# Optimization experiments

Measured on AMD Instinct MI355X. Metric: run time of the kernel, lower is better.

The kernel has to match this reference:

```python
import jax, jax.numpy as jnp
import numpy as np

E = 128
H = 4
D = E // H  # head dim = 32
NEG = -1e9


def setup_inputs() -> dict:
    key = jax.random.key(0)
    ks = jax.random.split(key, 4)
    B, N = 8, 2048
    x = jax.random.normal(ks[0], (B, N, E), dtype=jnp.float32)
    adj = jax.random.randint(ks[1], (B, N, N), 0, 2, dtype=jnp.int32)
    # nn.MultiheadAttention params: packed in_proj (3E,E) + out_proj (E,E)
    in_proj_w = jax.random.normal(ks[2], (3 * E, E), dtype=jnp.float32) * (1.0 / np.sqrt(E))
    in_proj_b = jnp.zeros((3 * E,), dtype=jnp.float32)
    out_w = jax.random.normal(ks[3], (E, E), dtype=jnp.float32) * (1.0 / np.sqrt(E))
    out_b = jnp.zeros((E,), dtype=jnp.float32)
    return {"x": x, "adj": adj, "in_proj_w": in_proj_w, "in_proj_b": in_proj_b,
            "out_w": out_w, "out_b": out_b}


def reference(x, adj, in_proj_w, in_proj_b, out_w, out_b):
    B, N, _ = x.shape
    # additive mask from FIRST batch element only (as in the torch module)
    mask = jnp.where(adj[0] == 0, jnp.float32(NEG), jnp.float32(0.0))  # (N,N)
    # packed QKV projection: x @ W^T + b
    qkv = x @ in_proj_w.T + in_proj_b  # (B,N,3E)
    q, k, v = jnp.split(qkv, 3, axis=-1)
    # (B,N,E) -> (B,H,N,D)
    def heads(t):
        return t.reshape(B, N, H, D).transpose(0, 2, 1, 3)
    q, k, v = heads(q), heads(k), heads(v)
    scores = jnp.einsum('bhnd,bhmd->bhnm', q, k) / jnp.sqrt(jnp.float32(D))
    scores = scores + mask[None, None]  # broadcast shared mask
    attn = jax.nn.softmax(scores, axis=-1)
    out = jnp.einsum('bhnm,bhmd->bhnd', attn, v)  # (B,H,N,D)
    out = out.transpose(0, 2, 1, 3).reshape(B, N, E)
    return out @ out_w.T + out_b
```

## Files before the change

### kernel.cpp

```cpp
#include <hip/hip_runtime.h>


#define EDIM 128
#define SCALE2 0.25503483f
#define COFF  -5.7707801f

typedef unsigned int uint32;
typedef float f32x4 __attribute__((ext_vector_type(4)));
typedef short s16x8 __attribute__((ext_vector_type(8)));
typedef _Float16 f16x2 __attribute__((ext_vector_type(2)));
typedef _Float16 f16x4 __attribute__((ext_vector_type(4)));
typedef _Float16 f16x8 __attribute__((ext_vector_type(8)));
typedef __fp16 g16x2 __attribute__((ext_vector_type(2)));

__device__ inline float bf2f(ushort u) { return __uint_as_float(((uint32)u) << 16); }
__device__ inline ushort f2bf(float f) {
  uint32 u = __float_as_uint(f);
  u += 0x7fffu + ((u >> 16) & 1u);
  return (ushort)(u >> 16);
}
__device__ inline uint32 packbf(float a, float b) {
  uint32 ua = __float_as_uint(a) + 0x8000u;
  uint32 ub = __float_as_uint(b) + 0x8000u;
  return __builtin_amdgcn_perm(ub, ua, 0x07060302u);
}
__device__ inline f16x2 pkrtz(float a, float b) {
  g16x2 t = __builtin_amdgcn_cvt_pkrtz(a, b);
  return __builtin_bit_cast(f16x2, t);
}
__device__ inline float fexp2(float x) {
#if __has_builtin(__builtin_amdgcn_exp2f)
  return __builtin_amdgcn_exp2f(x);
#else
  return __exp2f(x);
#endif
}

__device__ inline f32x4 mfma32(s16x8 a, s16x8 b, f32x4 c) {
  return __builtin_amdgcn_mfma_f32_16x16x32_bf16(a, b, c, 0, 0, 0);
}
__device__ inline f32x4 mfma32h(f16x8 a, f16x8 b, f32x4 c) {
  return __builtin_amdgcn_mfma_f32_16x16x32_f16(a, b, c, 0, 0, 0);
}

#if __has_builtin(__builtin_amdgcn_global_load_lds)
#define HAVE_GLL 1
__device__ inline void gll16(const void* g, void* l) {
  __builtin_amdgcn_global_load_lds(
      (const __attribute__((address_space(1))) unsigned int*)g,
      (__attribute__((address_space(3))) unsigned int*)l, 16, 0, 0);
}
#else
#define HAVE_GLL 0
#endif

__device__ inline int sniff_fp32(const ushort* __restrict__ xus) {
  int lane = threadIdx.x & 63, cnt = 0;
#pragma unroll
  for (int i = 0; i < 4; i++) {
    ushort v = xus[2 * (lane * 4 + i)];
    int ex = (v >> 7) & 0xFF;
    cnt += (ex >= 100 && ex <= 140) ? 1 : 0;
  }
#pragma unroll
  for (int s = 1; s < 64; s <<= 1) cnt += __shfl_xor(cnt, s);
  return cnt < 128;
}

__device__ inline s16x8 load8(const void* p, size_t e, int fp32) {
  if (fp32) {
    const float* f = (const float*)p + e;
    float4 lo = *(const float4*)f;
    float4 hi = *(const float4*)(f + 4);
    union { s16x8 s; uint32 u[4]; } r;
    r.u[0] = packbf(lo.x, lo.y);
    r.u[1] = packbf(lo.z, lo.w);
    r.u[2] = packbf(hi.x, hi.y);
    r.u[3] = packbf(hi.z, hi.w);
    return r.s;
  }
  return *(const s16x8*)((const ushort*)p + e);
}
__device__ inline float loads(const void* p, size_t e, int fp32) {
  return fp32 ? ((const float*)p)[e] : bf2f(((const ushort*)p)[e]);
}

__global__ __launch_bounds__(256) void k_mask(const int4* __restrict__ adj4,
                                              uint32* __restrict__ mb) {
  int g = blockIdx.x * 256 + threadIdx.x;
  int4 v = adj4[g];
  int lane = threadIdx.x & 63;
  uint32 nib = (v.x != 0 ? 1u : 0u) | (v.y != 0 ? 2u : 0u) |
               (v.z != 0 ? 4u : 0u) | (v.w != 0 ? 8u : 0u);
  uint32 w = nib << (4 * (lane & 7));
  w |= __shfl_xor(w, 1);
  w |= __shfl_xor(w, 2);
  w |= __shfl_xor(w, 4);
  if ((lane & 7) == 0) mb[g >> 3] = w;
}

__global__ __launch_bounds__(256) void k_qkv(const void* __restrict__ x,
                                             const void* __restrict__ w,
                                             const void* __restrict__ bias,
                                             ushort* __restrict__ Qg,
                                             ushort* __restrict__ Kg,
                                             _Float16* __restrict__ Vth) {
  const int fp32 = sniff_fp32((const ushort*)x);
  const int tid = threadIdx.x;
  const int wave = tid >> 6, lane = tid & 63, L = lane & 15, quad = lane >> 4;
  const int mt = blockIdx.x * 64 + wave * 16;
  const int jt0 = blockIdx.y * 8;

  s16x8 a[4];
#pragma unroll
  for (int ks = 0; ks < 4; ks++)
    a[ks] = load8(x, (size_t)(mt + L) * EDIM + ks * 32 + quad * 8, fp32);

  const int bidx = mt >> 11;
  const int npos0 = (mt & 2047) + quad * 4;

  for (int jj = 0; jj < 8; jj++) {
    int jt = jt0 + jj;
    f32x4 acc = {0.f, 0.f, 0.f, 0.f};
#pragma unroll
    for (int ks = 0; ks < 4; ks++) {
      s16x8 bf = load8(w, (size_t)(jt * 16 + L) * EDIM + ks * 32 + quad * 8, fp32);
      acc = mfma32(a[ks], bf, acc);
    }
    int j = jt * 16 + L;
    float badd = loads(bias, j, fp32);
    int jm = j & 127;
    int h = jm >> 5, d = jm & 31;
    int bh = bidx * 4 + h;
    int ch = npos0 >> 7, kk = npos0 & 127;
    if (jt < 8) {
#pragma unroll
      for (int r = 0; r < 4; r++)
        Qg[(size_t)bh * 65536 + (size_t)(npos0 + r) * 32 + d] = f2bf((acc[r] + badd) * SCALE2);
    } else if (jt < 16) {
      int sub = kk >> 5, k32 = kk & 31, t = k32 >> 3, r8 = k32 & 7;
      int slot0 = sub * 32 + ((r8 >> 2) << 4) + t * 4;
      size_t kb = (size_t)bh * 65536 + (size_t)ch * 4096;
#pragma unroll
      for (int r = 0; r < 4; r++)
        Kg[kb + (size_t)(slot0 + r) * 32 + (((d >> 3) ^ r) << 3) + (d & 7)] =
            f2bf(acc[r] + badd);
    } else {
      int g = kk >> 3, e0 = kk & 7;
      f16x2 h0 = pkrtz(acc[0] + badd, acc[1] + badd);
      f16x2 h1 = pkrtz(acc[2] + badd, acc[3] + badd);
      f16x4 pk; pk[0] = h0[0]; pk[1] = h0[1]; pk[2] = h1[0]; pk[3] = h1[1];
      *(f16x4*)(Vth + (size_t)bh * 65536 + (size_t)ch * 4096 + d * 128 +
                (g ^ (d & 7)) * 8 + e0) = pk;
    }
  }
}

__global__ __launch_bounds__(256) void k_attn(const ushort* __restrict__ Qg,
                                              const ushort* __restrict__ Kg,
                                              const _Float16* __restrict__ Vth,
                                              const uint32* __restrict__ mb,
                                              const ushort* __restrict__ xus,
                                              ushort* Oglob, ushort* Oa) {
  __shared__ ushort Klds[2][128 * 32];
  __shared__ ushort Vlds[2][32 * 128];

  const int fp32 = sniff_fp32(xus);
  ushort* O = fp32 ? Oa : Oglob;

  const int tid = threadIdx.x;
  const int wv = tid >> 6, lane = tid & 63, L = lane & 15, quad = lane >> 4;
  const int bh = blockIdx.x >> 4;
  const int q0 = (blockIdx.x & 15) * 128 + wv * 32;
  const int qgA = q0 + L, qgB = q0 + 16 + L;

  const ushort* Qb = Qg + (size_t)bh * 65536;
  s16x8 qfA = *(const s16x8*)(Qb + (size_t)qgA * 32 + quad * 8);
  s16x8 qfB = *(const s16x8*)(Qb + (size_t)qgB * 32 + quad * 8);

  f32x4 OA0 = {0,0,0,0}, OA1 = {0,0,0,0}, OB0 = {0,0,0,0}, OB1 = {0,0,0,0};
  f32x4 LA = {0,0,0,0}, LB = {0,0,0,0};
  f16x8 ones;
#pragma unroll
  for (int i = 0; i < 8; i++) ones[i] = (_Float16)1.0f;

  const char* Kg8 = (const char*)(Kg + (size_t)bh * 65536);
  const char* Vg8 = (const char*)(Vth + (size_t)bh * 65536);
  const int g0 = quad ^ (L & 3);

#define STAGE(c, p)                                                          \
  do {                                                                       \
    _Pragma("unroll")                                                        \
    for (int j = 0; j < 2; j++) {                                            \
      int off = (wv + 4 * j) * 1024;                                         \
      gll16(Kg8 + (size_t)(c) * 8192 + off + lane * 16, (char*)Klds[p] + off);\
      gll16(Vg8 + (size_t)(c) * 8192 + off + lane * 16, (char*)Vlds[p] + off);\
    }                                                                        \
  } while (0)

#if HAVE_GLL
  STAGE(0, 0);
#else
#pragma unroll
  for (int r = 0; r < 2; r++) {
    int idx = r * 256 + tid;
    *(s16x8*)((char*)Klds[0] + idx * 16) = *(const s16x8*)(Kg8 + idx * 16);
    *(s16x8*)((char*)Vlds[0] + idx * 16) = *(const s16x8*)(Vg8 + idx * 16);
  }
#endif

  for (int c = 0; c < 16; c++) {
    const int p = c & 1;
    __syncthreads();
#if HAVE_GLL
    if (c + 1 < 16) STAGE(c + 1, 1 - p);
#else
    if (c + 1 < 16) {
#pragma unroll
      for (int r = 0; r < 2; r++) {
        int idx = r * 256 + tid;
        *(s16x8*)((char*)Klds[1 - p] + idx * 16) =
            *(const s16x8*)(Kg8 + (size_t)(c + 1) * 8192 + idx * 16);
        *(s16x8*)((char*)Vlds[1 - p] + idx * 16) =
            *(const s16x8*)(Vg8 + (size_t)(c + 1) * 8192 + idx * 16);
      }
    }
#endif

    uint4 mA = *(const uint4*)(mb + (size_t)qgA * 64 + c * 4);
    uint4 mB = *(const uint4*)(mb + (size_t)qgB * 64 + c * 4);
    uint32 mAw[4] = {mA.x, mA.y, mA.z, mA.w};
    uint32 mBw[4] = {mB.x, mB.y, mB.z, mB.w};

#pragma unroll
    for (int sub = 0; sub < 4; sub++) {
      const f32x4 Zc = {COFF, COFF, COFF, COFF};
      s16x8 kf0 = *(const s16x8*)&Klds[p][(sub * 32 + L) * 32 + g0 * 8];
      s16x8 kf1 = *(const s16x8*)&Klds[p][(sub * 32 + 16 + L) * 32 + g0 * 8];
      f32x4 sA0 = mfma32(kf0, qfA, Zc), sA1 = mfma32(kf1, qfA, Zc);
      f32x4 sB0 = mfma32(kf0, qfB, Zc), sB1 = mfma32(kf1, qfB, Zc);

      uint32 mwqA = mAw[sub] >> (quad * 8);
      uint32 mwqB = mBw[sub] >> (quad * 8);
      union { f16x8 v; f16x2 h[4]; } pA, pB;
      float a0 = ((mwqA >> 0) & 1u) ? fexp2(sA0[0]) : 0.f;
      float a1 = ((mwqA >> 1) & 1u) ? fexp2(sA0[1]) : 0.f;
      float a2 = ((mwqA >> 2) & 1u) ? fexp2(sA0[2]) : 0.f;
      float a3 = ((mwqA >> 3) & 1u) ? fexp2(sA0[3]) : 0.f;
      float a4 = ((mwqA >> 4) & 1u) ? fexp2(sA1[0]) : 0.f;
      float a5 = ((mwqA >> 5) & 1u) ? fexp2(sA1[1]) : 0.f;
      float a6 = ((mwqA >> 6) & 1u) ? fexp2(sA1[2]) : 0.f;
      float a7 = ((mwqA >> 7) & 1u) ? fexp2(sA1[3]) : 0.f;
      pA.h[0] = pkrtz(a0, a1); pA.h[1] = pkrtz(a2, a3);
      pA.h[2] = pkrtz(a4, a5); pA.h[3] = pkrtz(a6, a7);
      float b0 = ((mwqB >> 0) & 1u) ? fexp2(sB0[0]) : 0.f;
      float b1 = ((mwqB >> 1) & 1u) ? fexp2(sB0[1]) : 0.f;
      float b2 = ((mwqB >> 2) & 1u) ? fexp2(sB0[2]) : 0.f;
      float b3 = ((mwqB >> 3) & 1u) ? fexp2(sB0[3]) : 0.f;
      float b4 = ((mwqB >> 4) & 1u) ? fexp2(sB1[0]) : 0.f;
      float b5 = ((mwqB >> 5) & 1u) ? fexp2(sB1[1]) : 0.f;
      float b6 = ((mwqB >> 6) & 1u) ? fexp2(sB1[2]) : 0.f;
      float b7 = ((mwqB >> 7) & 1u) ? fexp2(sB1[3]) : 0.f;
      pB.h[0] = pkrtz(b0, b1); pB.h[1] = pkrtz(b2, b3);
      pB.h[2] = pkrtz(b4, b5); pB.h[3] = pkrtz(b6, b7);

      int g = (sub * 4 + quad) ^ (L & 7);
      f16x8 vf0 = *(const f16x8*)&Vlds[p][L * 128 + g * 8];
      f16x8 vf1 = *(const f16x8*)&Vlds[p][(16 + L) * 128 + g * 8];
      OA0 = mfma32h(vf0, pA.v, OA0);  OA1 = mfma32h(vf1, pA.v, OA1);
      OB0 = mfma32h(vf0, pB.v, OB0);  OB1 = mfma32h(vf1, pB.v, OB1);
      LA  = mfma32h(ones, pA.v, LA);  LB  = mfma32h(ones, pB.v, LB);
    }
  }

  int b = bh >> 2, h = bh & 3;
  {
    float rn = 1.0f / LA[0];
    size_t ob = ((size_t)(b * 2048 + qgA)) * 128 + h * 32 + quad * 4;
    ushort4 p0, p1;
    p0.x = f2bf(OA0[0] * rn); p0.y = f2bf(OA0[1] * rn);
    p0.z = f2bf(OA0[2] * rn); p0.w = f2bf(OA0[3] * rn);
    p1.x = f2bf(OA1[0] * rn); p1.y = f2bf(OA1[1] * rn);
    p1.z = f2bf(OA1[2] * rn); p1.w = f2bf(OA1[3] * rn);
    *(ushort4*)(O + ob) = p0; *(ushort4*)(O + ob + 16) = p1;
  }
  {
    float rn = 1.0f / LB[0];
    size_t ob = ((size_t)(b * 2048 + qgB)) * 128 + h * 32 + quad * 4;
    ushort4 p0, p1;
    p0.x = f2bf(OB0[0] * rn); p0.y = f2bf(OB0[1] * rn);
    p0.z = f2bf(OB0[2] * rn); p0.w = f2bf(OB0[3] * rn);
    p1.x = f2bf(OB1[0] * rn); p1.y = f2bf(OB1[1] * rn);
    p1.z = f2bf(OB1[2] * rn); p1.w = f2bf(OB1[3] * rn);
    *(ushort4*)(O + ob) = p0; *(ushort4*)(O + ob + 16) = p1;
  }
}

__global__ __launch_bounds__(256) void k_proj(void* outp, const ushort* Oa,
                                              const void* w, const void* bias,
                                              const ushort* __restrict__ xus) {
  const int fp32 = sniff_fp32(xus);
  const ushort* src = fp32 ? Oa : (const ushort*)outp;
  const int tid = threadIdx.x;
  const int wave = tid >> 6, lane = tid & 63, L = lane & 15, quad = lane >> 4;
  const int mt = blockIdx.x * 64 + wave * 16;

  s16x8 a[4];
#pragma unroll
  for (int ks = 0; ks < 4; ks++)
    a[ks] = *(const s16x8*)(src + (size_t)(mt + L) * EDIM + ks * 32 + quad * 8);

  for (int jt = 0; jt < 8; jt++) {
    f32x4 acc = {0.f, 0.f, 0.f, 0.f};
#pragma unroll
    for (int ks = 0; ks < 4; ks++) {
      s16x8 bf = load8(w, (size_t)(jt * 16 + L) * EDIM + ks * 32 + quad * 8, fp32);
      acc = mfma32(a[ks], bf, acc);
    }
    float badd = loads(bias, jt * 16 + L, fp32);
#pragma unroll
    for (int r = 0; r < 4; r++) {
      size_t idx = (size_t)(mt + quad * 4 + r) * EDIM + jt * 16 + L;
      if (fp32) ((float*)outp)[idx] = acc[r] + badd;
      else      ((ushort*)outp)[idx] = f2bf(acc[r] + badd);
    }
  }
}

extern "C" void kernel_launch(void* const* d_in, const int* in_sizes, int n_in,
                              void* d_out, int out_size, void* d_ws, size_t ws_size,
                              hipStream_t stream) {
  const void* x   = d_in[0];
  const int*  adj = (const int*)d_in[1];
  const void* ipw = d_in[2];
  const void* ipb = d_in[3];
  const void* ow  = d_in[4];
  const void* ob  = d_in[5];

  char* ws = (char*)d_ws;
  ushort*   Qg  = (ushort*)(ws);
  ushort*   Kg  = (ushort*)(ws + ((size_t)4 << 20));
  _Float16* Vth = (_Float16*)(ws + ((size_t)8 << 20));
  uint32*   mb  = (uint32*)(ws + ((size_t)12 << 20));
  ushort*   Oa  = (ushort*)(ws + ((size_t)13 << 20));

  hipLaunchKernelGGL(k_mask, dim3(4096), dim3(256), 0, stream,
                     (const int4*)adj, mb);
  hipLaunchKernelGGL(k_qkv, dim3(256, 3), dim3(256), 0, stream, x, ipw, ipb,
                     Qg, Kg, Vth);
  hipLaunchKernelGGL(k_attn, dim3(512), dim3(256), 0, stream, Qg, Kg, Vth, mb,
                     (const ushort*)x, (ushort*)d_out, Oa);
  hipLaunchKernelGGL(k_proj, dim3(256), dim3(256), 0, stream, d_out, Oa, ow, ob,
                     (const ushort*)x);
}
```

Baseline: 269.5 us.

## Split attention KV range across two wave groups and parallelize output projection

The attention kernel now uses 512-thread blocks in which two groups of four waves each process half of the key/value sequence for the same query tile. Their partial outputs and row sums are combined through shared memory before normalization. The intermediate output always goes to the workspace buffer. The projection kernel splits its output columns across a second grid dimension to double the block count. This aims to raise occupancy on 256 CUs, where 512 blocks of 256 threads left the GPU underfilled, at the cost of a larger LDS footprint and an extra reduction with a barrier.

```diff
diff --git a/kernel.cpp b/kernel.cpp
--- a/kernel.cpp
+++ b/kernel.cpp
@@ -156,22 +156,19 @@
   }
 }
 
-__global__ __launch_bounds__(256) void k_attn(const ushort* __restrict__ Qg,
+__global__ __launch_bounds__(512) void k_attn(const ushort* __restrict__ Qg,
                                               const ushort* __restrict__ Kg,
                                               const _Float16* __restrict__ Vth,
                                               const uint32* __restrict__ mb,
-                                              const ushort* __restrict__ xus,
-                                              ushort* Oglob, ushort* Oa) {
-  __shared__ ushort Klds[2][128 * 32];
-  __shared__ ushort Vlds[2][32 * 128];
-
-  const int fp32 = sniff_fp32(xus);
-  ushort* O = fp32 ? Oa : Oglob;
+                                              ushort* __restrict__ Oa) {
+  __shared__ ushort Klds[2][2][128 * 32];
+  __shared__ ushort Vlds[2][2][32 * 128];
 
   const int tid = threadIdx.x;
   const int wv = tid >> 6, lane = tid & 63, L = lane & 15, quad = lane >> 4;
+  const int half = wv >> 2, wl = wv & 3;
   const int bh = blockIdx.x >> 4;
-  const int q0 = (blockIdx.x & 15) * 128 + wv * 32;
+  const int q0 = (blockIdx.x & 15) * 128 + wl * 32;
   const int qgA = q0 + L, qgB = q0 + 16 + L;
 
   const ushort* Qb = Qg + (size_t)bh * 65536;
@@ -184,49 +181,56 @@
 #pragma unroll
   for (int i = 0; i < 8; i++) ones[i] = (_Float16)1.0f;
 
-  const char* Kg8 = (const char*)(Kg + (size_t)bh * 65536);
-  const char* Vg8 = (const char*)(Vth + (size_t)bh * 65536);
+  const char* Kg8 = (const char*)(Kg + (size_t)bh * 65536) + (size_t)half * 65536;
+  const char* Vg8 = (const char*)(Vth + (size_t)bh * 65536) + (size_t)half * 65536;
   const int g0 = quad ^ (L & 3);
 
-#define STAGE(c, p)                                                          \
-  do {                                                                       \
-    _Pragma("unroll")                                                        \
-    for (int j = 0; j < 2; j++) {                                            \
-      int off = (wv + 4 * j) * 1024;                                         \
-      gll16(Kg8 + (size_t)(c) * 8192 + off + lane * 16, (char*)Klds[p] + off);\
-      gll16(Vg8 + (size_t)(c) * 8192 + off + lane * 16, (char*)Vlds[p] + off);\
-    }                                                                        \
+#define STAGE(cc, p)                                                          \
+  do {                                                                        \
+    _Pragma("unroll")                                                         \
+    for (int j = 0; j < 2; j++) {                                             \
+      int off = (wl + 4 * j) * 1024;                                          \
+      gll16(Kg8 + (size_t)(cc) * 8192 + off + lane * 16,                      \
+            (char*)Klds[half][p] + off);                                      \
+      gll16(Vg8 + (size_t)(cc) * 8192 + off + lane * 16,                      \
+            (char*)Vlds[half][p] + off);                                      \
+    }                                                                         \
   } while (0)
 
 #if HAVE_GLL
   STAGE(0, 0);
 #else
-#pragma unroll
-  for (int r = 0; r < 2; r++) {
-    int idx = r * 256 + tid;
-    *(s16x8*)((char*)Klds[0] + idx * 16) = *(const s16x8*)(Kg8 + idx * 16);
-    *(s16x8*)((char*)Vlds[0] + idx * 16) = *(const s16x8*)(Vg8 + idx * 16);
+  {
+    int t256 = tid & 255;
+#pragma unroll
+    for (int r = 0; r < 2; r++) {
+      int idx = r * 256 + t256;
+      *(s16x8*)((char*)Klds[half][0] + idx * 16) = *(const s16x8*)(Kg8 + idx * 16);
+      *(s16x8*)((char*)Vlds[half][0] + idx * 16) = *(const s16x8*)(Vg8 + idx * 16);
+    }
   }
 #endif
 
-  for (int c = 0; c < 16; c++) {
-    const int p = c & 1;
+  for (int cc = 0; cc < 8; cc++) {
+    const int p = cc & 1;
     __syncthreads();
 #if HAVE_GLL
-    if (c + 1 < 16) STAGE(c + 1, 1 - p);
+    if (cc + 1 < 8) STAGE(cc + 1, 1 - p);
 #else
-    if (c + 1 < 16) {
+    if (cc + 1 < 8) {
+      int t256 = tid & 255;
 #pragma unroll
       for (int r = 0; r < 2; r++) {
-        int idx = r * 256 + tid;
-        *(s16x8*)((char*)Klds[1 - p] + idx * 16) =
-            *(const s16x8*)(Kg8 + (size_t)(c + 1) * 8192 + idx * 16);
-        *(s16x8*)((char*)Vlds[1 - p] + idx * 16) =
-            *(const s16x8*)(Vg8 + (size_t)(c + 1) * 8192 + idx * 16);
+        int idx = r * 256 + t256;
+        *(s16x8*)((char*)Klds[half][1 - p] + idx * 16) =
+            *(const s16x8*)(Kg8 + (size_t)(cc + 1) * 8192 + idx * 16);
+        *(s16x8*)((char*)Vlds[half][1 - p] + idx * 16) =
+            *(const s16x8*)(Vg8 + (size_t)(cc + 1) * 8192 + idx * 16);
       }
     }
 #endif
 
+    const int c = half * 8 + cc;
     uint4 mA = *(const uint4*)(mb + (size_t)qgA * 64 + c * 4);
     uint4 mB = *(const uint4*)(mb + (size_t)qgB * 64 + c * 4);
     uint32 mAw[4] = {mA.x, mA.y, mA.z, mA.w};
@@ -235,8 +239,8 @@
 #pragma unroll
     for (int sub = 0; sub < 4; sub++) {
       const f32x4 Zc = {COFF, COFF, COFF, COFF};
-      s16x8 kf0 = *(const s16x8*)&Klds[p][(sub * 32 + L) * 32 + g0 * 8];
-      s16x8 kf1 = *(const s16x8*)&Klds[p][(sub * 32 + 16 + L) * 32 + g0 * 8];
+      s16x8 kf0 = *(const s16x8*)&Klds[half][p][(sub * 32 + L) * 32 + g0 * 8];
+      s16x8 kf1 = *(const s16x8*)&Klds[half][p][(sub * 32 + 16 + L) * 32 + g0 * 8];
       f32x4 sA0 = mfma32(kf0, qfA, Zc), sA1 = mfma32(kf1, qfA, Zc);
       f32x4 sB0 = mfma32(kf0, qfB, Zc), sB1 = mfma32(kf1, qfB, Zc);
 
@@ -265,34 +269,60 @@
       pB.h[2] = pkrtz(b4, b5); pB.h[3] = pkrtz(b6, b7);
 
       int g = (sub * 4 + quad) ^ (L & 7);
-      f16x8 vf0 = *(const f16x8*)&Vlds[p][L * 128 + g * 8];
-      f16x8 vf1 = *(const f16x8*)&Vlds[p][(16 + L) * 128 + g * 8];
+      f16x8 vf0 = *(const f16x8*)&Vlds[half][p][L * 128 + g * 8];
+      f16x8 vf1 = *(const f16x8*)&Vlds[half][p][(16 + L) * 128 + g * 8];
       OA0 = mfma32h(vf0, pA.v, OA0);  OA1 = mfma32h(vf1, pA.v, OA1);
       OB0 = mfma32h(vf0, pB.v, OB0);  OB1 = mfma32h(vf1, pB.v, OB1);
       LA  = mfma32h(ones, pA.v, LA);  LB  = mfma32h(ones, pB.v, LB);
     }
   }
 
-  int b = bh >> 2, h = bh & 3;
-  {
-    float rn = 1.0f / LA[0];
-    size_t ob = ((size_t)(b * 2048 + qgA)) * 128 + h * 32 + quad * 4;
-    ushort4 p0, p1;
-    p0.x = f2bf(OA0[0] * rn); p0.y = f2bf(OA0[1] * rn);
-    p0.z = f2bf(OA0[2] * rn); p0.w = f2bf(OA0[3] * rn);
-    p1.x = f2bf(OA1[0] * rn); p1.y = f2bf(OA1[1] * rn);
-    p1.z = f2bf(OA1[2] * rn); p1.w = f2bf(OA1[3] * rn);
-    *(ushort4*)(O + ob) = p0; *(ushort4*)(O + ob + 16) = p1;
-  }
-  {
-    float rn = 1.0f / LB[0];
-    size_t ob = ((size_t)(b * 2048 + qgB)) * 128 + h * 32 + quad * 4;
-    ushort4 p0, p1;
-    p0.x = f2bf(OB0[0] * rn); p0.y = f2bf(OB0[1] * rn);
-    p0.z = f2bf(OB0[2] * rn); p0.w = f2bf(OB0[3] * rn);
-    p1.x = f2bf(OB1[0] * rn); p1.y = f2bf(OB1[1] * rn);
-    p1.z = f2bf(OB1[2] * rn); p1.w = f2bf(OB1[3] * rn);
-    *(ushort4*)(O + ob) = p0; *(ushort4*)(O + ob + 16) = p1;
+  __syncthreads();
+  float* cb = (float*)&Klds[0][0][0];
+  const int cbase = wl * 1088;
+  if (half) {
+#pragma unroll
+    for (int r = 0; r < 4; r++) {
+      cb[cbase + L * 33 + quad * 4 + r]             = OA0[r];
+      cb[cbase + L * 33 + 16 + quad * 4 + r]        = OA1[r];
+      cb[cbase + (16 + L) * 33 + quad * 4 + r]      = OB0[r];
+      cb[cbase + (16 + L) * 33 + 16 + quad * 4 + r] = OB1[r];
+    }
+    if (quad == 0) {
+      cb[cbase + 1056 + L]      = LA[0];
+      cb[cbase + 1056 + 16 + L] = LB[0];
+    }
+  }
+  __syncthreads();
+  if (!half) {
+#pragma unroll
+    for (int r = 0; r < 4; r++) {
+      OA0[r] += cb[cbase + L * 33 + quad * 4 + r];
+      OA1[r] += cb[cbase + L * 33 + 16 + quad * 4 + r];
+      OB0[r] += cb[cbase + (16 + L) * 33 + quad * 4 + r];
+      OB1[r] += cb[cbase + (16 + L) * 33 + 16 + quad * 4 + r];
+    }
+    float rnA = 1.0f / (LA[0] + cb[cbase + 1056 + L]);
+    float rnB = 1.0f / (LB[0] + cb[cbase + 1056 + 16 + L]);
+    int b = bh >> 2, h = bh & 3;
+    {
+      size_t ob = ((size_t)(b * 2048 + qgA)) * 128 + h * 32 + quad * 4;
+      ushort4 p0, p1;
+      p0.x = f2bf(OA0[0] * rnA); p0.y = f2bf(OA0[1] * rnA);
+      p0.z = f2bf(OA0[2] * rnA); p0.w = f2bf(OA0[3] * rnA);
+      p1.x = f2bf(OA1[0] * rnA); p1.y = f2bf(OA1[1] * rnA);
+      p1.z = f2bf(OA1[2] * rnA); p1.w = f2bf(OA1[3] * rnA);
+      *(ushort4*)(Oa + ob) = p0; *(ushort4*)(Oa + ob + 16) = p1;
+    }
+    {
+      size_t ob = ((size_t)(b * 2048 + qgB)) * 128 + h * 32 + quad * 4;
+      ushort4 p0, p1;
+      p0.x = f2bf(OB0[0] * rnB); p0.y = f2bf(OB0[1] * rnB);
+      p0.z = f2bf(OB0[2] * rnB); p0.w = f2bf(OB0[3] * rnB);
+      p1.x = f2bf(OB1[0] * rnB); p1.y = f2bf(OB1[1] * rnB);
+      p1.z = f2bf(OB1[2] * rnB); p1.w = f2bf(OB1[3] * rnB);
+      *(ushort4*)(Oa + ob) = p0; *(ushort4*)(Oa + ob + 16) = p1;
+    }
   }
 }
 
@@ -300,17 +330,18 @@
                                               const void* w, const void* bias,
                                               const ushort* __restrict__ xus) {
   const int fp32 = sniff_fp32(xus);
-  const ushort* src = fp32 ? Oa : (const ushort*)outp;
+  const ushort* src = Oa;
   const int tid = threadIdx.x;
   const int wave = tid >> 6, lane = tid & 63, L = lane & 15, quad = lane >> 4;
   const int mt = blockIdx.x * 64 + wave * 16;
+  const int jt0 = blockIdx.y * 4;
 
   s16x8 a[4];
 #pragma unroll
   for (int ks = 0; ks < 4; ks++)
     a[ks] = *(const s16x8*)(src + (size_t)(mt + L) * EDIM + ks * 32 + quad * 8);
 
-  for (int jt = 0; jt < 8; jt++) {
+  for (int jt = jt0; jt < jt0 + 4; jt++) {
     f32x4 acc = {0.f, 0.f, 0.f, 0.f};
 #pragma unroll
     for (int ks = 0; ks < 4; ks++) {
@@ -348,8 +379,8 @@
                      (const int4*)adj, mb);
   hipLaunchKernelGGL(k_qkv, dim3(256, 3), dim3(256), 0, stream, x, ipw, ipb,
                      Qg, Kg, Vth);
-  hipLaunchKernelGGL(k_attn, dim3(512), dim3(256), 0, stream, Qg, Kg, Vth, mb,
-                     (const ushort*)x, (ushort*)d_out, Oa);
-  hipLaunchKernelGGL(k_proj, dim3(256), dim3(256), 0, stream, d_out, Oa, ow, ob,
+  hipLaunchKernelGGL(k_attn, dim3(512), dim3(512), 0, stream, Qg, Kg, Vth, mb,
+                     Oa);
+  hipLaunchKernelGGL(k_proj, dim3(256, 2), dim3(256), 0, stream, d_out, Oa, ow, ob,
                      (const ushort*)x);
 }
```

Result: faster. 254.9 us (-5.4%).
